# Kernel tuning notes

Hardware: AMD Instinct MI355X
Metric: run time of the kernel (lower is better)

## Reference

```python
import jax, jax.numpy as jnp
import numpy as np

T, B, IN, H, L = 512, 32, 320, 1024, 3
SLOPE, OFFSET = 0.2, 0.5
FORGET_BIAS = 1.0


def setup_inputs() -> dict:
    key = jax.random.key(0)
    ks = iter(jax.random.split(key, 64))
    stdv = 1.0 / np.sqrt(H)

    def u(k, shape):
        return jax.random.uniform(k, shape, jnp.float32, -stdv, stdv)

    inp = {
        "x": jax.random.normal(next(ks), (T, B, IN), jnp.float32),
        "h0": jnp.zeros((2 * L, B, H), jnp.float32),
        "c0": jnp.zeros((2 * L, B, H), jnp.float32),
    }
    for l in range(L):
        isz = IN if l == 0 else 2 * H
        for d in ("f", "r"):
            inp[f"w_ih_{l}{d}"] = u(next(ks), (4 * H, isz))
            inp[f"w_hh_{l}{d}"] = u(next(ks), (4 * H, H))
            b_ih = u(next(ks), (4 * H,))
            # forget_gate_bias: bias_ih forget slice set, bias_hh forget slice zeroed
            b_ih = b_ih.at[H:2 * H].set(FORGET_BIAS)
            b_hh = u(next(ks), (4 * H,))
            b_hh = b_hh.at[H:2 * H].set(0.0)
            inp[f"b_ih_{l}{d}"] = b_ih
            inp[f"b_hh_{l}{d}"] = b_hh
    return inp


def _hard_lstm_scan(x_seq, h, c, w_ih, w_hh, b):
    """x_seq: [T,B,I]; h,c: [B,H]. Returns ys [T,B,H], (h,c)."""
    # Batch the input-to-hidden GEMM across all timesteps.
    gx = jnp.einsum("tbi,gi->tbg", x_seq, w_ih) + b  # [T,B,4H]

    def step(carry, gxt):
        h, c = carry
        g = gxt + h @ w_hh.T
        i, f, gg, o = jnp.split(g, 4, axis=-1)
        i = jnp.clip(SLOPE * i + OFFSET, 0.0, 1.0)
        f = jnp.clip(SLOPE * f + OFFSET, 0.0, 1.0)
        gg = jnp.clip(gg, -1.0, 1.0)        # hardtanh
        o = jnp.clip(SLOPE * o + OFFSET, 0.0, 1.0)
        c = f * c + i * gg
        h = o * jnp.clip(c, -1.0, 1.0)
        return (h, c), h

    (h, c), ys = jax.lax.scan(step, (h, c), gx)
    return ys, h, c


def hard_lstm_forward(x, h0, c0, params):
    """params: list of L tuples ((fwd 4-tuple), (rev 4-tuple))."""
    y = x
    for l, (pf, pr) in enumerate(params):
        w_ih_f, w_hh_f, b_ih_f, b_hh_f = pf
        w_ih_r, w_hh_r, b_ih_r, b_hh_r = pr
        yf, _, _ = _hard_lstm_scan(y, h0[2 * l], c0[2 * l], w_ih_f, w_hh_f, b_ih_f + b_hh_f)
        yr, _, _ = _hard_lstm_scan(y[::-1], h0[2 * l + 1], c0[2 * l + 1], w_ih_r, w_hh_r, b_ih_r + b_hh_r)
        y = jnp.concatenate([yf, yr[::-1]], axis=-1)  # [T,B,2H]
    return y


def reference(x, h0, c0,
              w_ih_0f, w_hh_0f, b_ih_0f, b_hh_0f,
              w_ih_0r, w_hh_0r, b_ih_0r, b_hh_0r,
              w_ih_1f, w_hh_1f, b_ih_1f, b_hh_1f,
              w_ih_1r, w_hh_1r, b_ih_1r, b_hh_1r,
              w_ih_2f, w_hh_2f, b_ih_2f, b_hh_2f,
              w_ih_2r, w_hh_2r, b_ih_2r, b_hh_2r):
    params = [
        ((w_ih_0f, w_hh_0f, b_ih_0f, b_hh_0f), (w_ih_0r, w_hh_0r, b_ih_0r, b_hh_0r)),
        ((w_ih_1f, w_hh_1f, b_ih_1f, b_hh_1f), (w_ih_1r, w_hh_1r, b_ih_1r, b_hh_1r)),
        ((w_ih_2f, w_hh_2f, b_ih_2f, b_hh_2f), (w_ih_2r, w_hh_2r, b_ih_2r, b_hh_2r)),
    ]
    return hard_lstm_forward(x, h0, c0, params)
```

## Files before the change

kernel.cpp:

```cpp
#include <hip/hip_runtime.h>

typedef __attribute__((ext_vector_type(8))) short short8;
typedef __attribute__((ext_vector_type(4))) short short4v;
typedef __attribute__((ext_vector_type(4))) float f32x4;
typedef unsigned long long u64;

__device__ __forceinline__ short f2bf(float x) {
  union { float f; unsigned u; } v; v.f = x;
  unsigned r = v.u + 0x7fffu + ((v.u >> 16) & 1u);
  return (short)(r >> 16);
}
__device__ __forceinline__ float bf2f(short b) {
  union { unsigned u; float f; } v; v.u = ((unsigned)(unsigned short)b) << 16;
  return v.f;
}

#define GLOAD_LDS16(g, l) __builtin_amdgcn_global_load_lds( \
    (const __attribute__((address_space(1))) void*)(g),     \
    (__attribute__((address_space(3))) void*)(l), 16, 0, 0)

__global__ void k_cvt(const float* __restrict__ s, short* __restrict__ d, int n) {
  int stride = gridDim.x * blockDim.x * 4;
  for (int i = (blockIdx.x * blockDim.x + threadIdx.x) * 4; i < n; i += stride) {
    float4 v = *(const float4*)(s + i);
    short4v o;
    o.x = f2bf(v.x); o.y = f2bf(v.y); o.z = f2bf(v.z); o.w = f2bf(v.w);
    *(short4v*)(d + i) = o;
  }
}

__global__ void k_bias(const float* __restrict__ bif, const float* __restrict__ bhf,
                       const float* __restrict__ bir, const float* __restrict__ bhr,
                       float* __restrict__ o) {
  int i = blockIdx.x * 256 + threadIdx.x;
  o[i] = (i < 4096) ? (bif[i] + bhf[i]) : (bir[i - 4096] + bhr[i - 4096]);
}

__global__ void k_zero(int* __restrict__ p) { p[blockIdx.x * 256 + threadIdx.x] = 0; }

__global__ void __launch_bounds__(256) k_gemm(
    const short* __restrict__ A, const short* __restrict__ Bt,
    const float* __restrict__ bias, short* __restrict__ C,
    int M, int N, int K)
{
  __shared__ short Al[128 * 64];
  __shared__ short Bl[128 * 64];
  const int nm = M >> 7;
  int wg = blockIdx.x;
  int q = gridDim.x >> 3;
  wg = (wg & 7) * q + (wg >> 3);
  const int mt = wg % nm, nt = wg / nm;
  const int tid = threadIdx.x, lane = tid & 63, w = tid >> 6;
  const int wr = w >> 1, wc = w & 1;
  const short* Ab = A + (size_t)(mt * 128) * K;
  const short* Bb = Bt + (size_t)(nt * 128) * K;
  f32x4 acc[4][4] = {};
  const int lrow = lane >> 3, lseg = lane & 7;

  for (int kt = 0; kt < K; kt += 64) {
#pragma unroll
    for (int s = 0; s < 4; ++s) {
      int chunk = s * 4 + w;
      int r = chunk * 8 + lrow;
      GLOAD_LDS16(Ab + (size_t)r * K + kt + lseg * 8, &Al[chunk * 512]);
      GLOAD_LDS16(Bb + (size_t)r * K + kt + lseg * 8, &Bl[chunk * 512]);
    }
    __syncthreads();
#pragma unroll
    for (int kk = 0; kk < 2; ++kk) {
      short8 af[4], bfr[4];
#pragma unroll
      for (int i = 0; i < 4; ++i) {
        af[i]  = *(const short8*)&Al[(wr * 64 + i * 16 + (lane & 15)) * 64 + kk * 32 + (lane >> 4) * 8];
        bfr[i] = *(const short8*)&Bl[(wc * 64 + i * 16 + (lane & 15)) * 64 + kk * 32 + (lane >> 4) * 8];
      }
#pragma unroll
      for (int i = 0; i < 4; ++i)
#pragma unroll
        for (int j = 0; j < 4; ++j)
          acc[i][j] = __builtin_amdgcn_mfma_f32_16x16x32_bf16(af[i], bfr[j], acc[i][j], 0, 0, 0);
    }
    __syncthreads();
  }

  const int r0 = mt * 128 + wr * 64, c0n = nt * 128 + wc * 64;
#pragma unroll
  for (int i = 0; i < 4; ++i) {
#pragma unroll
    for (int j = 0; j < 4; ++j) {
      int col = c0n + j * 16 + (lane & 15);
      float bv = bias[col];
#pragma unroll
      for (int r = 0; r < 4; ++r) {
        int row = r0 + i * 16 + (lane >> 4) * 4 + r;
        C[(size_t)row * N + col] = f2bf(acc[i][j][r] + bv);
      }
    }
  }
}

template <bool LAST>
__global__ void __launch_bounds__(512, 1) k_scan(
    const short* __restrict__ gx,
    const short* __restrict__ whh,
    const float* __restrict__ h0,
    const float* __restrict__ c0,
    short* __restrict__ hbuf,
    void* __restrict__ yout,
    int layer, int* __restrict__ bar)
{
  const int tid = threadIdx.x, lane = tid & 63, kq = tid >> 6;
  const int dir = blockIdx.x >> 6, wid = blockIdx.x & 63;
  const int hc0 = wid * 16;
  extern __shared__ float part[];
  int* seq = bar + dir * 64 * 32;

  short8 wfr[16];
#pragma unroll
  for (int ni = 0; ni < 4; ++ni) {
    const int l15 = lane & 15;
    const int grow = dir * 4096 + ni * 1024 + hc0 + l15;
    const short* wp = whh + (size_t)grow * 1024 + kq * 128 + (lane >> 4) * 8;
#pragma unroll
    for (int ks = 0; ks < 4; ++ks) wfr[ni * 4 + ks] = *(const short8*)(wp + ks * 32);
  }
#pragma unroll
  for (int i = 0; i < 16; ++i) asm volatile("" : "+v"(wfr[i]));

  const int b4 = tid >> 2, cg = tid & 3, col0 = hc0 + cg * 4;
  float ca[4] = {0.f, 0.f, 0.f, 0.f};
  short4v pgi, pgf, pgg, pgo;
  if (tid < 128) {
    const int sidx = ((2 * layer + dir) * 32 + b4) * 1024 + col0;
    float4 cv = *(const float4*)(c0 + sidx);
    ca[0] = cv.x; ca[1] = cv.y; ca[2] = cv.z; ca[3] = cv.w;
    float4 hv = *(const float4*)(h0 + sidx);
    union { u64 u; short s[4]; } pk;
    pk.s[0] = f2bf(hv.x); pk.s[1] = f2bf(hv.y); pk.s[2] = f2bf(hv.z); pk.s[3] = f2bf(hv.w);
    size_t qi = (size_t)dir * 8192 + (size_t)b4 * 256 + wid * 4 + cg;
    __hip_atomic_store((u64*)hbuf + qi, pk.u,
                       __ATOMIC_RELAXED, __HIP_MEMORY_SCOPE_AGENT);
    asm volatile("s_waitcnt vmcnt(0)" ::: "memory");
  }
  __syncthreads();
  if (tid == 0)
    __hip_atomic_store(seq + wid * 32, 1, __ATOMIC_RELAXED, __HIP_MEMORY_SCOPE_AGENT);
  if (tid < 128) {
    const int t0 = dir ? 511 : 0;
    const short* gp = gx + ((size_t)(t0 * 32 + b4)) * 8192 + dir * 4096 + col0;
    pgi = *(const short4v*)(gp);
    pgf = *(const short4v*)(gp + 1024);
    pgg = *(const short4v*)(gp + 2048);
    pgo = *(const short4v*)(gp + 3072);
  }

  int p = 0;
  for (int ts = 0; ts < 512; ++ts) {
    const int t = dir ? (511 - ts) : ts;

    if (lane < 8) {
      int* sp = seq + (kq * 8 + lane) * 32;
      while (__hip_atomic_load(sp, __ATOMIC_RELAXED, __HIP_MEMORY_SCOPE_AGENT) < ts + 1)
        __builtin_amdgcn_s_sleep(1);
    }
    asm volatile("" ::: "memory");
    __syncthreads();

    u64* hb = (u64*)hbuf + (size_t)(p * 2 + dir) * 8192;
    short8 af[8];
#pragma unroll
    for (int mi = 0; mi < 2; ++mi) {
      const size_t rb = (size_t)(mi * 16 + (lane & 15)) * 256 + kq * 32 + (lane >> 4) * 2;
#pragma unroll
      for (int ks = 0; ks < 4; ++ks) {
        union { u64 u[2]; short8 v; } tu;
        tu.u[0] = __hip_atomic_load(hb + rb + ks * 8,     __ATOMIC_RELAXED, __HIP_MEMORY_SCOPE_AGENT);
        tu.u[1] = __hip_atomic_load(hb + rb + ks * 8 + 1, __ATOMIC_RELAXED, __HIP_MEMORY_SCOPE_AGENT);
        af[mi * 4 + ks] = tu.v;
      }
    }
#pragma unroll
    for (int i = 0; i < 8; ++i) asm volatile("" : "+v"(af[i]));

    f32x4 acc[2][4] = {};
#pragma unroll
    for (int ks = 0; ks < 4; ++ks) {
#pragma unroll
      for (int mi = 0; mi < 2; ++mi)
#pragma unroll
        for (int ni = 0; ni < 4; ++ni)
          acc[mi][ni] = __builtin_amdgcn_mfma_f32_16x16x32_bf16(
              af[mi * 4 + ks], wfr[ni * 4 + ks], acc[mi][ni], 0, 0, 0);
    }
#pragma unroll
    for (int mi = 0; mi < 2; ++mi)
#pragma unroll
      for (int ni = 0; ni < 4; ++ni)
#pragma unroll
        for (int r = 0; r < 4; ++r)
          part[(kq * 64 + ni * 16 + (lane & 15)) * 35 + mi * 16 + (lane >> 4) * 4 + r] = acc[mi][ni][r];
    __syncthreads();

    union { u64 u; short s[4]; } pk;
    float hv[4];
    if (tid < 128) {
      const int c7 = cg * 4;
#pragma unroll
      for (int j = 0; j < 4; ++j) {
        float gi = bf2f(pgi[j]), gf = bf2f(pgf[j]), gg = bf2f(pgg[j]), go = bf2f(pgo[j]);
#pragma unroll
        for (int q = 0; q < 8; ++q) {
          gi += part[(q * 64      + c7 + j) * 35 + b4];
          gf += part[(q * 64 + 16 + c7 + j) * 35 + b4];
          gg += part[(q * 64 + 32 + c7 + j) * 35 + b4];
          go += part[(q * 64 + 48 + c7 + j) * 35 + b4];
        }
        float i_ = fminf(fmaxf(0.2f * gi + 0.5f, 0.f), 1.f);
        float f_ = fminf(fmaxf(0.2f * gf + 0.5f, 0.f), 1.f);
        float g_ = fminf(fmaxf(gg, -1.f), 1.f);
        float o_ = fminf(fmaxf(0.2f * go + 0.5f, 0.f), 1.f);
        float cc = f_ * ca[j] + i_ * g_;
        ca[j] = cc;
        hv[j] = o_ * fminf(fmaxf(cc, -1.f), 1.f);
        pk.s[j] = f2bf(hv[j]);
      }
      size_t qi = (size_t)((p ^ 1) * 2 + dir) * 8192 + (size_t)b4 * 256 + wid * 4 + cg;
      __hip_atomic_store((u64*)hbuf + qi, pk.u,
                         __ATOMIC_RELAXED, __HIP_MEMORY_SCOPE_AGENT);
      asm volatile("s_waitcnt vmcnt(0)" ::: "memory");
    }
    __syncthreads();
    if (tid == 0)
      __hip_atomic_store(seq + wid * 32, ts + 2, __ATOMIC_RELAXED, __HIP_MEMORY_SCOPE_AGENT);
    if (tid < 128) {
      size_t yi = ((size_t)(t * 32 + b4)) * 2048 + dir * 1024 + col0;
      if (LAST) {
        float4 f4; f4.x = hv[0]; f4.y = hv[1]; f4.z = hv[2]; f4.w = hv[3];
        *(float4*)((float*)yout + yi) = f4;
      } else {
        short4v ys; ys.x = pk.s[0]; ys.y = pk.s[1]; ys.z = pk.s[2]; ys.w = pk.s[3];
        *(short4v*)((short*)yout + yi) = ys;
      }
      if (ts < 511) {
        const int tn = dir ? (511 - (ts + 1)) : (ts + 1);
        const short* gp = gx + ((size_t)(tn * 32 + b4)) * 8192 + dir * 4096 + col0;
        pgi = *(const short4v*)(gp);
        pgf = *(const short4v*)(gp + 1024);
        pgg = *(const short4v*)(gp + 2048);
        pgo = *(const short4v*)(gp + 3072);
      }
    }
    p ^= 1;
  }
}

extern "C" void kernel_launch(void* const* d_in, const int* in_sizes, int n_in,
                              void* d_out, int out_size, void* d_ws, size_t ws_size,
                              hipStream_t stream)
{
  const float* x  = (const float*)d_in[0];
  const float* h0 = (const float*)d_in[1];
  const float* c0 = (const float*)d_in[2];
  auto W = [&](int l, int d, int k) { return (const float*)d_in[3 + l * 8 + d * 4 + k]; };

  char* base = (char*)d_ws;
  size_t off = 0;
  auto alloc = [&](size_t bytes) {
    void* p = base + off;
    off = (off + bytes + 255) & ~(size_t)255;
    return p;
  };
  short* xb    = (short*)alloc(16384ull * 320 * 2);
  short* wih0  = (short*)alloc(8192ull * 320 * 2);
  short* wih1  = (short*)alloc(8192ull * 2048 * 2);
  short* wih2  = (short*)alloc(8192ull * 2048 * 2);
  short* whh0  = (short*)alloc(8192ull * 1024 * 2);
  short* whh1  = (short*)alloc(8192ull * 1024 * 2);
  short* whh2  = (short*)alloc(8192ull * 1024 * 2);
  float* bias0 = (float*)alloc(8192ull * 4);
  float* bias1 = (float*)alloc(8192ull * 4);
  float* bias2 = (float*)alloc(8192ull * 4);
  short* gx    = (short*)alloc(16384ull * 8192 * 2);
  short* y1    = (short*)alloc(16384ull * 2048 * 2);
  short* y2    = (short*)alloc(16384ull * 2048 * 2);
  short* hbuf  = (short*)alloc(2ull * 2 * 32 * 1024 * 2);
  int*   bar   = (int*)alloc(2ull * 64 * 32 * 4);
  (void)ws_size; (void)in_sizes; (void)n_in; (void)out_size;

  auto cvt = [&](const float* s, short* d, size_t n) {
    size_t want = (n / 4 + 255) / 256;
    int blocks = (int)(want > 2048 ? 2048 : want);
    k_cvt<<<dim3(blocks), dim3(256), 0, stream>>>(s, d, (int)n);
  };

  cvt(x, xb, 16384ull * 320);
  short* wihs[3] = { wih0, wih1, wih2 };
  short* whhs[3] = { whh0, whh1, whh2 };
  float* biases[3] = { bias0, bias1, bias2 };
  for (int l = 0; l < 3; ++l) {
    size_t kin = (l == 0) ? 320 : 2048;
    cvt(W(l, 0, 0), wihs[l],                  4096 * kin);
    cvt(W(l, 1, 0), wihs[l] + 4096 * kin,     4096 * kin);
    cvt(W(l, 0, 1), whhs[l],                  4096ull * 1024);
    cvt(W(l, 1, 1), whhs[l] + 4096ull * 1024, 4096ull * 1024);
    k_bias<<<dim3(32), dim3(256), 0, stream>>>(W(l, 0, 2), W(l, 0, 3), W(l, 1, 2), W(l, 1, 3), biases[l]);
  }

  const int M = 16384, N = 8192;
  const int LDSB = 8 * 64 * 35 * 4;

  k_gemm<<<dim3((M / 128) * (N / 128)), dim3(256), 0, stream>>>(xb, wih0, bias0, gx, M, N, 320);
  k_zero<<<dim3(16), dim3(256), 0, stream>>>(bar);
  k_scan<false><<<dim3(128), dim3(512), LDSB, stream>>>(gx, whh0, h0, c0, hbuf, (void*)y1, 0, bar);
  k_gemm<<<dim3((M / 128) * (N / 128)), dim3(256), 0, stream>>>(y1, wih1, bias1, gx, M, N, 2048);
  k_zero<<<dim3(16), dim3(256), 0, stream>>>(bar);
  k_scan<false><<<dim3(128), dim3(512), LDSB, stream>>>(gx, whh1, h0, c0, hbuf, (void*)y2, 1, bar);
  k_gemm<<<dim3((M / 128) * (N / 128)), dim3(256), 0, stream>>>(y2, wih2, bias2, gx, M, N, 2048);
  k_zero<<<dim3(16), dim3(256), 0, stream>>>(bar);
  k_scan<true><<<dim3(128), dim3(512), LDSB, stream>>>(gx, whh2, h0, c0, hbuf, d_out, 2, bar);
}
```

Before: 11.99 ms.

## Replace per-block sequence counters with tagged hidden-state words for scan sync

The recurrent scan kernel no longer uses separate per-workgroup sequence counters plus a block barrier to signal that a new hidden state is ready. Each 64-bit word of the hidden-state exchange buffer now carries a 16-bit timestep tag alongside 48 bits of bf16 data, and consumers spin on the data loads themselves until every tag matches. This removes the waitcnt, the extra syncthreads and the counter round-trip on the critical path of each timestep. In exchange the buffer grows by half, each read needs three loads and some unpacking, and polling now rereads the full hidden-state slice on every retry.

```diff
diff --git a/kernel.cpp b/kernel.cpp
--- a/kernel.cpp
+++ b/kernel.cpp
@@ -36,7 +36,7 @@
   o[i] = (i < 4096) ? (bif[i] + bhf[i]) : (bir[i - 4096] + bhr[i - 4096]);
 }
 
-__global__ void k_zero(int* __restrict__ p) { p[blockIdx.x * 256 + threadIdx.x] = 0; }
+__global__ void k_zero_h(u64* __restrict__ p) { p[blockIdx.x * 256 + threadIdx.x] = 0; }
 
 __global__ void __launch_bounds__(256) k_gemm(
     const short* __restrict__ A, const short* __restrict__ Bt,
@@ -105,21 +105,19 @@
     const short* __restrict__ whh,
     const float* __restrict__ h0,
     const float* __restrict__ c0,
-    short* __restrict__ hbuf,
+    u64* __restrict__ hbuf,
     void* __restrict__ yout,
-    int layer, int* __restrict__ bar)
+    int layer)
 {
   const int tid = threadIdx.x, lane = tid & 63, kq = tid >> 6;
   const int dir = blockIdx.x >> 6, wid = blockIdx.x & 63;
   const int hc0 = wid * 16;
   extern __shared__ float part[];
-  int* seq = bar + dir * 64 * 32;
 
   short8 wfr[16];
 #pragma unroll
   for (int ni = 0; ni < 4; ++ni) {
-    const int l15 = lane & 15;
-    const int grow = dir * 4096 + ni * 1024 + hc0 + l15;
+    const int grow = dir * 4096 + ni * 1024 + hc0 + (lane & 15);
     const short* wp = whh + (size_t)grow * 1024 + kq * 128 + (lane >> 4) * 8;
 #pragma unroll
     for (int ks = 0; ks < 4; ++ks) wfr[ni * 4 + ks] = *(const short8*)(wp + ks * 32);
@@ -128,6 +126,7 @@
   for (int i = 0; i < 16; ++i) asm volatile("" : "+v"(wfr[i]));
 
   const int b4 = tid >> 2, cg = tid & 3, col0 = hc0 + cg * 4;
+  const int g_own = wid * 2 + (cg >> 1);
   float ca[4] = {0.f, 0.f, 0.f, 0.f};
   short4v pgi, pgf, pgg, pgo;
   if (tid < 128) {
@@ -137,15 +136,18 @@
     float4 hv = *(const float4*)(h0 + sidx);
     union { u64 u; short s[4]; } pk;
     pk.s[0] = f2bf(hv.x); pk.s[1] = f2bf(hv.y); pk.s[2] = f2bf(hv.z); pk.s[3] = f2bf(hv.w);
-    size_t qi = (size_t)dir * 8192 + (size_t)b4 * 256 + wid * 4 + cg;
-    __hip_atomic_store((u64*)hbuf + qi, pk.u,
-                       __ATOMIC_RELAXED, __HIP_MEMORY_SCOPE_AGENT);
-    asm volatile("s_waitcnt vmcnt(0)" ::: "memory");
-  }
-  __syncthreads();
-  if (tid == 0)
-    __hip_atomic_store(seq + wid * 32, 1, __ATOMIC_RELAXED, __HIP_MEMORY_SCOPE_AGENT);
-  if (tid < 128) {
+    unsigned oddlo = (unsigned)__shfl_xor((int)(unsigned)pk.u, 1);
+    const u64 tagw = 1ull << 48;
+    u64* wb = hbuf + (size_t)(1 * 2 + dir) * 12288 + ((size_t)b4 * 128 + g_own) * 3;
+    if ((cg & 1) == 0) {
+      __hip_atomic_store(wb,     (pk.u & 0x0000ffffffffffffull) | tagw,
+                         __ATOMIC_RELAXED, __HIP_MEMORY_SCOPE_AGENT);
+      __hip_atomic_store(wb + 1, (pk.u >> 48) | ((u64)oddlo << 16) | tagw,
+                         __ATOMIC_RELAXED, __HIP_MEMORY_SCOPE_AGENT);
+    } else {
+      __hip_atomic_store(wb + 2, ((pk.u >> 32) & 0xffffffffull) | tagw,
+                         __ATOMIC_RELAXED, __HIP_MEMORY_SCOPE_AGENT);
+    }
     const int t0 = dir ? 511 : 0;
     const short* gp = gx + ((size_t)(t0 * 32 + b4)) * 8192 + dir * 4096 + col0;
     pgi = *(const short4v*)(gp);
@@ -154,33 +156,40 @@
     pgo = *(const short4v*)(gp + 3072);
   }
 
-  int p = 0;
   for (int ts = 0; ts < 512; ++ts) {
     const int t = dir ? (511 - ts) : ts;
 
-    if (lane < 8) {
-      int* sp = seq + (kq * 8 + lane) * 32;
-      while (__hip_atomic_load(sp, __ATOMIC_RELAXED, __HIP_MEMORY_SCOPE_AGENT) < ts + 1)
+    short8 af[8];
+    {
+      const unsigned tg = (unsigned)(ts + 1);
+      const u64* hbp = hbuf + (size_t)(((ts + 1) & 1) * 2 + dir) * 12288;
+      while (true) {
+        int ok = 1;
+#pragma unroll
+        for (int mi = 0; mi < 2; ++mi) {
+#pragma unroll
+          for (int ks = 0; ks < 4; ++ks) {
+            const int row = mi * 16 + (lane & 15);
+            const int g   = kq * 16 + ks * 4 + (lane >> 4);
+            const u64* wp = hbp + ((size_t)row * 128 + g) * 3;
+            u64 q0 = __hip_atomic_load(wp,     __ATOMIC_RELAXED, __HIP_MEMORY_SCOPE_AGENT);
+            u64 q1 = __hip_atomic_load(wp + 1, __ATOMIC_RELAXED, __HIP_MEMORY_SCOPE_AGENT);
+            u64 q2 = __hip_atomic_load(wp + 2, __ATOMIC_RELAXED, __HIP_MEMORY_SCOPE_AGENT);
+            ok &= (int)(((unsigned)(q0 >> 48) == tg) & ((unsigned)(q1 >> 48) == tg) &
+                        ((unsigned)(q2 >> 48) == tg));
+            union { unsigned u[4]; short8 v; } fu;
+            unsigned b0 = (unsigned)q1;
+            fu.u[0] = (unsigned)q0;
+            fu.u[1] = ((unsigned)(q0 >> 32) & 0xffffu) | (b0 << 16);
+            fu.u[2] = (b0 >> 16) | ((unsigned)(q1 >> 32) << 16);
+            fu.u[3] = (unsigned)q2;
+            af[mi * 4 + ks] = fu.v;
+          }
+        }
+        if (__all(ok)) break;
         __builtin_amdgcn_s_sleep(1);
-    }
-    asm volatile("" ::: "memory");
-    __syncthreads();
-
-    u64* hb = (u64*)hbuf + (size_t)(p * 2 + dir) * 8192;
-    short8 af[8];
-#pragma unroll
-    for (int mi = 0; mi < 2; ++mi) {
-      const size_t rb = (size_t)(mi * 16 + (lane & 15)) * 256 + kq * 32 + (lane >> 4) * 2;
-#pragma unroll
-      for (int ks = 0; ks < 4; ++ks) {
-        union { u64 u[2]; short8 v; } tu;
-        tu.u[0] = __hip_atomic_load(hb + rb + ks * 8,     __ATOMIC_RELAXED, __HIP_MEMORY_SCOPE_AGENT);
-        tu.u[1] = __hip_atomic_load(hb + rb + ks * 8 + 1, __ATOMIC_RELAXED, __HIP_MEMORY_SCOPE_AGENT);
-        af[mi * 4 + ks] = tu.v;
-      }
-    }
-#pragma unroll
-    for (int i = 0; i < 8; ++i) asm volatile("" : "+v"(af[i]));
+      }
+    }
 
     f32x4 acc[2][4] = {};
 #pragma unroll
@@ -201,10 +210,10 @@
           part[(kq * 64 + ni * 16 + (lane & 15)) * 35 + mi * 16 + (lane >> 4) * 4 + r] = acc[mi][ni][r];
     __syncthreads();
 
-    union { u64 u; short s[4]; } pk;
-    float hv[4];
     if (tid < 128) {
       const int c7 = cg * 4;
+      float hv[4];
+      union { u64 u; short s[4]; } pk;
 #pragma unroll
       for (int j = 0; j < 4; ++j) {
         float gi = bf2f(pgi[j]), gf = bf2f(pgf[j]), gg = bf2f(pgg[j]), go = bf2f(pgo[j]);
@@ -224,15 +233,19 @@
         hv[j] = o_ * fminf(fmaxf(cc, -1.f), 1.f);
         pk.s[j] = f2bf(hv[j]);
       }
-      size_t qi = (size_t)((p ^ 1) * 2 + dir) * 8192 + (size_t)b4 * 256 + wid * 4 + cg;
-      __hip_atomic_store((u64*)hbuf + qi, pk.u,
-                         __ATOMIC_RELAXED, __HIP_MEMORY_SCOPE_AGENT);
-      asm volatile("s_waitcnt vmcnt(0)" ::: "memory");
-    }
-    __syncthreads();
-    if (tid == 0)
-      __hip_atomic_store(seq + wid * 32, ts + 2, __ATOMIC_RELAXED, __HIP_MEMORY_SCOPE_AGENT);
-    if (tid < 128) {
+      const unsigned tp = (unsigned)(ts + 2);
+      const u64 tagw = (u64)tp << 48;
+      unsigned oddlo = (unsigned)__shfl_xor((int)(unsigned)pk.u, 1);
+      u64* wb = hbuf + (size_t)((tp & 1) * 2 + dir) * 12288 + ((size_t)b4 * 128 + g_own) * 3;
+      if ((cg & 1) == 0) {
+        __hip_atomic_store(wb,     (pk.u & 0x0000ffffffffffffull) | tagw,
+                           __ATOMIC_RELAXED, __HIP_MEMORY_SCOPE_AGENT);
+        __hip_atomic_store(wb + 1, (pk.u >> 48) | ((u64)oddlo << 16) | tagw,
+                           __ATOMIC_RELAXED, __HIP_MEMORY_SCOPE_AGENT);
+      } else {
+        __hip_atomic_store(wb + 2, ((pk.u >> 32) & 0xffffffffull) | tagw,
+                           __ATOMIC_RELAXED, __HIP_MEMORY_SCOPE_AGENT);
+      }
       size_t yi = ((size_t)(t * 32 + b4)) * 2048 + dir * 1024 + col0;
       if (LAST) {
         float4 f4; f4.x = hv[0]; f4.y = hv[1]; f4.z = hv[2]; f4.w = hv[3];
@@ -250,7 +263,7 @@
         pgo = *(const short4v*)(gp + 3072);
       }
     }
-    p ^= 1;
+    __syncthreads();
   }
 }
 
@@ -283,8 +296,7 @@
   short* gx    = (short*)alloc(16384ull * 8192 * 2);
   short* y1    = (short*)alloc(16384ull * 2048 * 2);
   short* y2    = (short*)alloc(16384ull * 2048 * 2);
-  short* hbuf  = (short*)alloc(2ull * 2 * 32 * 1024 * 2);
-  int*   bar   = (int*)alloc(2ull * 64 * 32 * 4);
+  u64*   hbuf  = (u64*)alloc(4ull * 12288 * 8);
   (void)ws_size; (void)in_sizes; (void)n_in; (void)out_size;
 
   auto cvt = [&](const float* s, short* d, size_t n) {
@@ -310,12 +322,12 @@
   const int LDSB = 8 * 64 * 35 * 4;
 
   k_gemm<<<dim3((M / 128) * (N / 128)), dim3(256), 0, stream>>>(xb, wih0, bias0, gx, M, N, 320);
-  k_zero<<<dim3(16), dim3(256), 0, stream>>>(bar);
-  k_scan<false><<<dim3(128), dim3(512), LDSB, stream>>>(gx, whh0, h0, c0, hbuf, (void*)y1, 0, bar);
+  k_zero_h<<<dim3(192), dim3(256), 0, stream>>>(hbuf);
+  k_scan<false><<<dim3(128), dim3(512), LDSB, stream>>>(gx, whh0, h0, c0, hbuf, (void*)y1, 0);
   k_gemm<<<dim3((M / 128) * (N / 128)), dim3(256), 0, stream>>>(y1, wih1, bias1, gx, M, N, 2048);
-  k_zero<<<dim3(16), dim3(256), 0, stream>>>(bar);
-  k_scan<false><<<dim3(128), dim3(512), LDSB, stream>>>(gx, whh1, h0, c0, hbuf, (void*)y2, 1, bar);
+  k_zero_h<<<dim3(192), dim3(256), 0, stream>>>(hbuf);
+  k_scan<false><<<dim3(128), dim3(512), LDSB, stream>>>(gx, whh1, h0, c0, hbuf, (void*)y2, 1);
   k_gemm<<<dim3((M / 128) * (N / 128)), dim3(256), 0, stream>>>(y2, wih2, bias2, gx, M, N, 2048);
-  k_zero<<<dim3(16), dim3(256), 0, stream>>>(bar);
-  k_scan<true><<<dim3(128), dim3(512), LDSB, stream>>>(gx, whh2, h0, c0, hbuf, d_out, 2, bar);
-}
+  k_zero_h<<<dim3(192), dim3(256), 0, stream>>>(hbuf);
+  k_scan<true><<<dim3(128), dim3(512), LDSB, stream>>>(gx, whh2, h0, c0, hbuf, d_out, 2);
+}
```

After: 17.81 ms. 48.5% more time.
